# Optimization experiments

Hardware: AMD Instinct MI355X
Metric: run time of the kernel (lower is better)

The kernel has to match this reference:

```python
import jax, jax.numpy as jnp
import numpy as np

MARGIN = 1.0

def _safe_sqrt(x):
    # sqrt with zero gradient at x<=0 (matches relu().sqrt() forward; avoids NaN grads on the zero diagonal)
    pos = x > 0
    return jnp.where(pos, jnp.sqrt(jnp.where(pos, x, 1.0)), 0.0)

def _smoothed_metric_loss(X, m=MARGIN):
    # X: [N, d], N even; lifted-structure smoothed loss (Song et al.)
    N = X.shape[0]
    sq = jnp.sum(X * X, axis=1)                       # [N]
    G = X @ X.T                                       # [N, N]
    D = _safe_sqrt(jax.nn.relu(sq[:, None] + sq[None, :] - 2.0 * G))
    E = jnp.exp(m - D)                                # [N, N]
    P = N // 2
    i = jnp.arange(P) * 2
    j = i + 1
    # negatives for pair p: rows {i,j}, all cols except {i,j}
    row_pair_sum = E.reshape(P, 2, N).sum(axis=(1, 2))  # [P] = rowsum(i)+rowsum(j)
    excl = E[i, i] + E[i, j] + E[j, i] + E[j, j]
    neg_sum = row_pair_sum - excl
    J = jnp.log(neg_sum) + D[i, j]
    return jnp.sum(jax.nn.relu(J) ** 2) / (2.0 * P)

def reference(text_embeddings, shape_embeddings):
    N = text_embeddings.shape[0]
    # tt loss on text embeddings
    metric_tt = _smoothed_metric_loss(text_embeddings, MARGIN)
    # repeat each shape embedding twice (index_select with i//2)
    shape_rep = jnp.repeat(shape_embeddings, 2, axis=0)  # [N, d]
    mask = jnp.tile(jnp.array([1.0, 0.0], dtype=text_embeddings.dtype), N // 2)[:, None]
    inv = 1.0 - mask
    e1 = text_embeddings * mask + shape_rep * inv
    e2 = text_embeddings * inv + shape_rep * mask
    emb = jnp.concatenate([e1, e2], axis=0)              # [2N, d]
    metric_st = _smoothed_metric_loss(emb, MARGIN)
    return metric_tt + metric_st

def setup_inputs() -> dict:
    key = jax.random.key(0)
    k1, k2 = jax.random.split(key)
    N, Dim = 4096, 256
    text = jax.random.normal(k1, (N, Dim), dtype=jnp.float32)
    shape = jax.random.normal(k2, (N // 2, Dim), dtype=jnp.float32)
    return {"text_embeddings": text, "shape_embeddings": shape}
```

## Files before the change

kernel.cpp:

```cpp
#include <hip/hip_runtime.h>
#include <hip/hip_bf16.h>
#include <math.h>


typedef __bf16 bf16x8 __attribute__((ext_vector_type(8)));
typedef float floatx4 __attribute__((ext_vector_type(4)));

#define KD 256
#define NU 6144
#define NBU 48
#define TU (NBU * (NBU + 1) / 2)
#define BM 128
#define BK 32
#define KSTEPS (KD / BK)
#define ECONST 2.718281828459045f

#define LSLOT(r, q) ((((r) * 4 + ((q) ^ (((r) >> 1) & 3)))) * 8)

__device__ __forceinline__ void gload_lds16(const void* g, void* l) {
  __builtin_amdgcn_global_load_lds((const __attribute__((address_space(1))) unsigned int*)g,
                                   (__attribute__((address_space(3))) unsigned int*)l,
                                   16, 0, 0);
}

__global__ __launch_bounds__(256) void prep_kernel(const float* __restrict__ text,
                                                   const float* __restrict__ shape,
                                                   __bf16* __restrict__ Xu,
                                                   float* __restrict__ sq,
                                                   float* __restrict__ rowacc,
                                                   float* __restrict__ out, int out_n) {
  int gt = blockIdx.x * 256 + threadIdx.x;
  if (gt < 2 * NU) rowacc[gt] = 0.f;
  if (gt < out_n) out[gt] = 0.f;
  int wave = gt >> 6;
  int lane = gt & 63;
  const float* src = (wave < 4096) ? (text + (size_t)wave * KD)
                                   : (shape + (size_t)(wave - 4096) * KD);
  float4 v = ((const float4*)src)[lane];
  __bf16 h0 = (__bf16)v.x, h1 = (__bf16)v.y, h2 = (__bf16)v.z, h3 = (__bf16)v.w;
  union { __bf16 h[4]; ushort2 u2[2]; } pk;
  pk.h[0] = h0; pk.h[1] = h1; pk.h[2] = h2; pk.h[3] = h3;
  ((ushort2*)(Xu + (size_t)wave * KD))[lane * 2] = pk.u2[0];
  ((ushort2*)(Xu + (size_t)wave * KD))[lane * 2 + 1] = pk.u2[1];
  float f0 = (float)h0, f1 = (float)h1, f2 = (float)h2, f3 = (float)h3;
  float s = f0 * f0 + f1 * f1 + f2 * f2 + f3 * f3;
#pragma unroll
  for (int m = 1; m < 64; m <<= 1) s += __shfl_xor(s, m, 64);
  if (lane == 0) sq[wave] = s;
}

__global__ __launch_bounds__(256, 3) void egemm_tri_kernel(
    const __bf16* __restrict__ X, const float* __restrict__ sq,
    float* __restrict__ rowacc) {
  __shared__ __align__(16) __bf16 As[3][BM * BK];
  __shared__ __align__(16) __bf16 Bs[3][BM * BK];
  __shared__ float rowbuf[2][128];
  __shared__ float colbuf[2][128];

  int t = blockIdx.x;
  int by = (int)((sqrtf(8.0f * (float)t + 1.0f) - 1.0f) * 0.5f);
  while ((by + 1) * (by + 2) / 2 <= t) ++by;
  while (by * (by + 1) / 2 > t) --by;
  const int bx = t - by * (by + 1) / 2;

  const int mBase = by * BM;
  const int nBase = bx * BM;
  const bool diag = (by == bx);

  const int tid = threadIdx.x;
  const int lane = tid & 63;
  const int w = tid >> 6;
  const int warpM = w >> 1, warpN = w & 1;
  const int quad = lane >> 4;
  const int l15 = lane & 15;

  floatx4 acc[4][4] = {};

  const int sRow = lane >> 2;
  const int sCol = (((lane & 3) ^ ((lane >> 3) & 3))) * 8;

#define STAGE(b, kt)                                                                   \
  {                                                                                    \
    _Pragma("unroll") for (int h = 0; h < 2; ++h) {                                    \
      int c = h * 4 + w;                                                               \
      gload_lds16(X + (size_t)(mBase + c * 16 + sRow) * KD + (kt) + sCol,              \
                  &As[b][c * 512]);                                                    \
      gload_lds16(X + (size_t)(nBase + c * 16 + sRow) * KD + (kt) + sCol,              \
                  &Bs[b][c * 512]);                                                    \
    }                                                                                  \
  }

  STAGE(0, 0);
  STAGE(1, BK);
#pragma unroll
  for (int s = 0; s < KSTEPS; ++s) {
    if (s < KSTEPS - 1)
      asm volatile("s_waitcnt vmcnt(4)" ::: "memory");
    else
      asm volatile("s_waitcnt vmcnt(0)" ::: "memory");
    __builtin_amdgcn_s_barrier();
    asm volatile("" ::: "memory");
    if (s + 2 < KSTEPS) STAGE((s + 2) % 3, (s + 2) * BK);

    const int cur = s % 3;
    bf16x8 af[4], bfr[4];
#pragma unroll
    for (int tm = 0; tm < 4; ++tm)
      af[tm] = *(const bf16x8*)&As[cur][LSLOT(warpM * 64 + tm * 16 + l15, quad)];
#pragma unroll
    for (int tn = 0; tn < 4; ++tn)
      bfr[tn] = *(const bf16x8*)&Bs[cur][LSLOT(warpN * 64 + tn * 16 + l15, quad)];
#pragma unroll
    for (int tm = 0; tm < 4; ++tm)
#pragma unroll
      for (int tn = 0; tn < 4; ++tn)
        acc[tm][tn] = __builtin_amdgcn_mfma_f32_16x16x32_bf16(af[tm], bfr[tn], acc[tm][tn], 0, 0, 0);
  }
#undef STAGE

  const int rbase = mBase + warpM * 64;
  const int cbase = nBase + warpN * 64;
  float sqr[4][4], sqc[4];
#pragma unroll
  for (int tm = 0; tm < 4; ++tm)
#pragma unroll
    for (int r = 0; r < 4; ++r)
      sqr[tm][r] = sq[rbase + tm * 16 + quad * 4 + r];
#pragma unroll
  for (int tn = 0; tn < 4; ++tn)
    sqc[tn] = sq[cbase + tn * 16 + l15];

  const float L2E = 1.44269504088896f;
  float cs[4] = {0.f, 0.f, 0.f, 0.f};
#pragma unroll
  for (int tm = 0; tm < 4; ++tm) {
    float rs[4] = {0.f, 0.f, 0.f, 0.f};
#pragma unroll
    for (int tn = 0; tn < 4; ++tn) {
#pragma unroll
      for (int r = 0; r < 4; ++r) {
        float v = acc[tm][tn][r];
        float dsq = fmaf(-2.0f, v, sqr[tm][r] + sqc[tn]);
        float dst = sqrtf(fmaxf(dsq, 0.f));
        float ev = __builtin_amdgcn_exp2f(fmaf(-L2E, dst, L2E));
        if (diag && tm == tn && (quad * 4 + r) == l15) ev = 0.f;
        rs[r] += ev;
        cs[tn] += ev;
      }
    }
#pragma unroll
    for (int r = 0; r < 4; ++r) {
      float v = rs[r];
      v += __shfl_xor(v, 1, 64);
      v += __shfl_xor(v, 2, 64);
      v += __shfl_xor(v, 4, 64);
      v += __shfl_xor(v, 8, 64);
      if (l15 == 0) rowbuf[warpN][warpM * 64 + tm * 16 + quad * 4 + r] = v;
    }
  }
#pragma unroll
  for (int tn = 0; tn < 4; ++tn) {
    float v = cs[tn];
    v += __shfl_xor(v, 16, 64);
    v += __shfl_xor(v, 32, 64);
    if (quad == 0) colbuf[warpM][warpN * 64 + tn * 16 + l15] = v;
  }
  __syncthreads();

  float* rdst = rowacc + (bx < 32 ? 0 : NU);
  float* cdst = rowacc + (by < 32 ? 0 : NU);
  if (tid < 128) {
    atomicAdd(&rdst[mBase + tid], rowbuf[0][tid] + rowbuf[1][tid]);
  } else if (!diag) {
    int c = tid - 128;
    atomicAdd(&cdst[nBase + c], colbuf[0][c] + colbuf[1][c]);
  }
}

__global__ __launch_bounds__(256) void loss_kernel(const float* __restrict__ text,
                                                   const float* __restrict__ shape,
                                                   const float* __restrict__ rowacc,
                                                   float* __restrict__ out) {
  __shared__ float part[4];
  const float* St = rowacc;
  const float* Ss = rowacc + NU;
  const int w = threadIdx.x >> 6;
  const int lane = threadIdx.x & 63;
  float jacc = 0.f;
#pragma unroll
  for (int it = 0; it < 2; ++it) {
    int wv = it * 3072 + blockIdx.x * 4 + w;
    const float *a, *b;
    float base, scale;
    if (wv < 2048) {
      int p = wv;
      a = text + (size_t)(2 * p) * KD;
      b = text + (size_t)(2 * p + 1) * KD;
      base = St[2 * p] + St[2 * p + 1];
      scale = 1.0f / 4096.0f;
    } else {
      int p = wv - 2048;
      int u1, u2;
      if (p < 2048) {
        u1 = 2 * p; u2 = 4096 + p;
        a = text + (size_t)(2 * p) * KD;
        b = shape + (size_t)p * KD;
      } else {
        int s = p - 2048;
        u1 = 4096 + s; u2 = 2 * s + 1;
        a = shape + (size_t)s * KD;
        b = text + (size_t)(2 * s + 1) * KD;
      }
      float g1 = St[u1] + 2.0f * Ss[u1];
      float g2 = St[u2] + 2.0f * Ss[u2];
      base = g1 + g2 + ECONST;
      scale = 1.0f / 8192.0f;
    }
    float4 va = ((const float4*)a)[lane];
    float4 vb = ((const float4*)b)[lane];
    float d0 = va.x - vb.x, d1 = va.y - vb.y, d2 = va.z - vb.z, d3 = va.w - vb.w;
    float s = d0 * d0 + d1 * d1 + d2 * d2 + d3 * d3;
#pragma unroll
    for (int m = 1; m < 64; m <<= 1) s += __shfl_xor(s, m, 64);
    if (lane == 0) {
      float D = s > 0.f ? sqrtf(s) : 0.f;
      float ns = base - 2.0f * expf(1.0f - D);
      float J = logf(ns) + D;
      jacc += (J > 0.f) ? J * J * scale : 0.f;
    }
  }
  if (lane == 0) part[w] = jacc;
  __syncthreads();
  if (threadIdx.x == 0) atomicAdd(out, part[0] + part[1] + part[2] + part[3]);
}

extern "C" void kernel_launch(void* const* d_in, const int* in_sizes, int n_in,
                              void* d_out, int out_size, void* d_ws, size_t ws_size,
                              hipStream_t stream) {
  const float* text = (const float*)d_in[0];
  const float* shape = (const float*)d_in[1];
  float* out = (float*)d_out;

  char* ws = (char*)d_ws;
  __bf16* Xu = (__bf16*)ws;
  float* sq = (float*)(ws + (size_t)NU * KD * 2);
  float* rowacc = sq + NU;

  prep_kernel<<<NU / 4, 256, 0, stream>>>(text, shape, Xu, sq, rowacc, out, out_size);
  egemm_tri_kernel<<<TU, 256, 0, stream>>>(Xu, sq, rowacc);
  loss_kernel<<<768, 256, 0, stream>>>(text, shape, rowacc, out);
}
```

Before: 100.4 us.

## Process two triangular tiles per block, prefetching second tile during first epilogue

Each block now computes two consecutive lower-triangular output tiles, running a single 16-step K loop where the second tile's loads are issued while the first tile is finishing and its exp/row-sum epilogue runs. This hides the global-load prologue of the second tile behind epilogue math and halves the number of blocks launched. It adds register pressure from keeping two sets of squared-norm values and may change occupancy and tail balance.

```diff
diff --git a/kernel.cpp b/kernel.cpp
--- a/kernel.cpp
+++ b/kernel.cpp
@@ -12,7 +12,6 @@
 #define TU (NBU * (NBU + 1) / 2)
 #define BM 128
 #define BK 32
-#define KSTEPS (KD / BK)
 #define ECONST 2.718281828459045f
 
 #define LSLOT(r, q) ((((r) * 4 + ((q) ^ (((r) >> 1) & 3)))) * 8)
@@ -49,87 +48,11 @@
   if (lane == 0) sq[wave] = s;
 }
 
-__global__ __launch_bounds__(256, 3) void egemm_tri_kernel(
-    const __bf16* __restrict__ X, const float* __restrict__ sq,
+__device__ __forceinline__ void tile_epilogue(
+    const floatx4 (&acc)[4][4], const float (&sqr)[4][4], const float (&sqc)[4],
+    bool diag, int mBase, int nBase, int by, int bx, int tid, int quad, int l15,
+    int warpM, int warpN, float (*rowbuf)[128], float (*colbuf)[128],
     float* __restrict__ rowacc) {
-  __shared__ __align__(16) __bf16 As[3][BM * BK];
-  __shared__ __align__(16) __bf16 Bs[3][BM * BK];
-  __shared__ float rowbuf[2][128];
-  __shared__ float colbuf[2][128];
-
-  int t = blockIdx.x;
-  int by = (int)((sqrtf(8.0f * (float)t + 1.0f) - 1.0f) * 0.5f);
-  while ((by + 1) * (by + 2) / 2 <= t) ++by;
-  while (by * (by + 1) / 2 > t) --by;
-  const int bx = t - by * (by + 1) / 2;
-
-  const int mBase = by * BM;
-  const int nBase = bx * BM;
-  const bool diag = (by == bx);
-
-  const int tid = threadIdx.x;
-  const int lane = tid & 63;
-  const int w = tid >> 6;
-  const int warpM = w >> 1, warpN = w & 1;
-  const int quad = lane >> 4;
-  const int l15 = lane & 15;
-
-  floatx4 acc[4][4] = {};
-
-  const int sRow = lane >> 2;
-  const int sCol = (((lane & 3) ^ ((lane >> 3) & 3))) * 8;
-
-#define STAGE(b, kt)                                                                   \
-  {                                                                                    \
-    _Pragma("unroll") for (int h = 0; h < 2; ++h) {                                    \
-      int c = h * 4 + w;                                                               \
-      gload_lds16(X + (size_t)(mBase + c * 16 + sRow) * KD + (kt) + sCol,              \
-                  &As[b][c * 512]);                                                    \
-      gload_lds16(X + (size_t)(nBase + c * 16 + sRow) * KD + (kt) + sCol,              \
-                  &Bs[b][c * 512]);                                                    \
-    }                                                                                  \
-  }
-
-  STAGE(0, 0);
-  STAGE(1, BK);
-#pragma unroll
-  for (int s = 0; s < KSTEPS; ++s) {
-    if (s < KSTEPS - 1)
-      asm volatile("s_waitcnt vmcnt(4)" ::: "memory");
-    else
-      asm volatile("s_waitcnt vmcnt(0)" ::: "memory");
-    __builtin_amdgcn_s_barrier();
-    asm volatile("" ::: "memory");
-    if (s + 2 < KSTEPS) STAGE((s + 2) % 3, (s + 2) * BK);
-
-    const int cur = s % 3;
-    bf16x8 af[4], bfr[4];
-#pragma unroll
-    for (int tm = 0; tm < 4; ++tm)
-      af[tm] = *(const bf16x8*)&As[cur][LSLOT(warpM * 64 + tm * 16 + l15, quad)];
-#pragma unroll
-    for (int tn = 0; tn < 4; ++tn)
-      bfr[tn] = *(const bf16x8*)&Bs[cur][LSLOT(warpN * 64 + tn * 16 + l15, quad)];
-#pragma unroll
-    for (int tm = 0; tm < 4; ++tm)
-#pragma unroll
-      for (int tn = 0; tn < 4; ++tn)
-        acc[tm][tn] = __builtin_amdgcn_mfma_f32_16x16x32_bf16(af[tm], bfr[tn], acc[tm][tn], 0, 0, 0);
-  }
-#undef STAGE
-
-  const int rbase = mBase + warpM * 64;
-  const int cbase = nBase + warpN * 64;
-  float sqr[4][4], sqc[4];
-#pragma unroll
-  for (int tm = 0; tm < 4; ++tm)
-#pragma unroll
-    for (int r = 0; r < 4; ++r)
-      sqr[tm][r] = sq[rbase + tm * 16 + quad * 4 + r];
-#pragma unroll
-  for (int tn = 0; tn < 4; ++tn)
-    sqc[tn] = sq[cbase + tn * 16 + l15];
-
   const float L2E = 1.44269504088896f;
   float cs[4] = {0.f, 0.f, 0.f, 0.f};
 #pragma unroll
@@ -166,7 +89,6 @@
     if (quad == 0) colbuf[warpM][warpN * 64 + tn * 16 + l15] = v;
   }
   __syncthreads();
-
   float* rdst = rowacc + (bx < 32 ? 0 : NU);
   float* cdst = rowacc + (by < 32 ? 0 : NU);
   if (tid < 128) {
@@ -175,6 +97,115 @@
     int c = tid - 128;
     atomicAdd(&cdst[nBase + c], colbuf[0][c] + colbuf[1][c]);
   }
+}
+
+__global__ __launch_bounds__(256, 3) void egemm_tri_kernel(
+    const __bf16* __restrict__ X, const float* __restrict__ sq,
+    float* __restrict__ rowacc) {
+  __shared__ __align__(16) __bf16 As[3][BM * BK];
+  __shared__ __align__(16) __bf16 Bs[3][BM * BK];
+  __shared__ float rowbuf[2][128];
+  __shared__ float colbuf[2][128];
+
+  const int t0 = blockIdx.x * 2;
+  int by0 = (int)((sqrtf(8.0f * (float)t0 + 1.0f) - 1.0f) * 0.5f);
+  while ((by0 + 1) * (by0 + 2) / 2 <= t0) ++by0;
+  while (by0 * (by0 + 1) / 2 > t0) --by0;
+  const int bx0 = t0 - by0 * (by0 + 1) / 2;
+  int by1, bx1;
+  if (bx0 < by0) { by1 = by0; bx1 = bx0 + 1; }
+  else           { by1 = by0 + 1; bx1 = 0;   }
+
+  const int mB0 = by0 * BM, nB0 = bx0 * BM;
+  const int mB1 = by1 * BM, nB1 = bx1 * BM;
+  const bool dg0 = (by0 == bx0), dg1 = (by1 == bx1);
+
+  const int tid = threadIdx.x;
+  const int lane = tid & 63;
+  const int w = tid >> 6;
+  const int warpM = w >> 1, warpN = w & 1;
+  const int quad = lane >> 4;
+  const int l15 = lane & 15;
+  const int sRow = lane >> 2;
+  const int sCol = (((lane & 3) ^ ((lane >> 3) & 3))) * 8;
+
+  float sqr0[4][4], sqc0[4], sqr1[4][4], sqc1[4];
+  {
+    const int rb = mB0 + warpM * 64, cb = nB0 + warpN * 64;
+#pragma unroll
+    for (int tm = 0; tm < 4; ++tm)
+#pragma unroll
+      for (int r = 0; r < 4; ++r) sqr0[tm][r] = sq[rb + tm * 16 + quad * 4 + r];
+#pragma unroll
+    for (int tn = 0; tn < 4; ++tn) sqc0[tn] = sq[cb + tn * 16 + l15];
+  }
+
+  floatx4 acc[4][4] = {};
+
+#define STAGE(buf, MB, NB, kt)                                                         \
+  {                                                                                    \
+    _Pragma("unroll") for (int h = 0; h < 2; ++h) {                                    \
+      int c = h * 4 + w;                                                               \
+      gload_lds16(X + (size_t)((MB) + c * 16 + sRow) * KD + (kt) + sCol,               \
+                  &As[buf][c * 512]);                                                  \
+      gload_lds16(X + (size_t)((NB) + c * 16 + sRow) * KD + (kt) + sCol,               \
+                  &Bs[buf][c * 512]);                                                  \
+    }                                                                                  \
+  }
+
+  STAGE(0, mB0, nB0, 0);
+  STAGE(1, mB0, nB0, BK);
+
+  for (int g = 0; g < 16; ++g) {
+    if (g == 8) {
+      {
+        const int rb = mB1 + warpM * 64, cb = nB1 + warpN * 64;
+#pragma unroll
+        for (int tm = 0; tm < 4; ++tm)
+#pragma unroll
+          for (int r = 0; r < 4; ++r) sqr1[tm][r] = sq[rb + tm * 16 + quad * 4 + r];
+#pragma unroll
+        for (int tn = 0; tn < 4; ++tn) sqc1[tn] = sq[cb + tn * 16 + l15];
+      }
+      tile_epilogue(acc, sqr0, sqc0, dg0, mB0, nB0, by0, bx0, tid, quad, l15,
+                    warpM, warpN, rowbuf, colbuf, rowacc);
+#pragma unroll
+      for (int tm = 0; tm < 4; ++tm)
+#pragma unroll
+        for (int tn = 0; tn < 4; ++tn)
+#pragma unroll
+          for (int r = 0; r < 4; ++r) acc[tm][tn][r] = 0.f;
+    }
+    if (g == 8 || g == 15)
+      asm volatile("s_waitcnt vmcnt(0)" ::: "memory");
+    else
+      asm volatile("s_waitcnt vmcnt(4)" ::: "memory");
+    __builtin_amdgcn_s_barrier();
+    asm volatile("" ::: "memory");
+    if (g + 2 < 8) {
+      STAGE((g + 2) % 3, mB0, nB0, (g + 2) * BK);
+    } else if (g + 2 < 16) {
+      STAGE((g + 2) % 3, mB1, nB1, ((g + 2) & 7) * BK);
+    }
+
+    const int cur = g % 3;
+    bf16x8 af[4], bfr[4];
+#pragma unroll
+    for (int tm = 0; tm < 4; ++tm)
+      af[tm] = *(const bf16x8*)&As[cur][LSLOT(warpM * 64 + tm * 16 + l15, quad)];
+#pragma unroll
+    for (int tn = 0; tn < 4; ++tn)
+      bfr[tn] = *(const bf16x8*)&Bs[cur][LSLOT(warpN * 64 + tn * 16 + l15, quad)];
+#pragma unroll
+    for (int tm = 0; tm < 4; ++tm)
+#pragma unroll
+      for (int tn = 0; tn < 4; ++tn)
+        acc[tm][tn] = __builtin_amdgcn_mfma_f32_16x16x32_bf16(af[tm], bfr[tn], acc[tm][tn], 0, 0, 0);
+  }
+#undef STAGE
+
+  tile_epilogue(acc, sqr1, sqc1, dg1, mB1, nB1, by1, bx1, tid, quad, l15,
+                warpM, warpN, rowbuf, colbuf, rowacc);
 }
 
 __global__ __launch_bounds__(256) void loss_kernel(const float* __restrict__ text,
@@ -247,6 +278,6 @@
   float* rowacc = sq + NU;
 
   prep_kernel<<<NU / 4, 256, 0, stream>>>(text, shape, Xu, sq, rowacc, out, out_size);
-  egemm_tri_kernel<<<TU, 256, 0, stream>>>(Xu, sq, rowacc);
+  egemm_tri_kernel<<<TU / 2, 256, 0, stream>>>(Xu, sq, rowacc);
   loss_kernel<<<768, 256, 0, stream>>>(text, shape, rowacc, out);
 }
```

Result: slower. 145.1 us (+44.6%).
